# Kernel optimization log

Measured on AMD Instinct MI355X. Metric: run time of the kernel, lower is better.

Reference implementation:

```python
import jax, jax.numpy as jnp
import numpy as np

# Static configuration (matches init_kwargs)
EMBED_DIM = 256
NUM_HEADS = 8
NUM_LEVELS = 4
NUM_POINTS = 16
N_DEGREE = 3
HEAD_DIM = EMBED_DIM // NUM_HEADS
SPATIAL_SHAPES = ((64, 64), (32, 32), (16, 16), (8, 8))  # (H, W) per level
LEN_V = sum(h * w for h, w in SPATIAL_SHAPES)


def _bilinear_gather(v, loc, Hl, Wl):
    """Bilinear sampling with zero padding, align_corners=False.
    v:   [bs, nH, Hl*Wl, hd]  flattened level feature map (per head)
    loc: [bs, nH, Q, 2]       (x, y) in [0, 1]
    returns [bs, nH, Q, hd]
    """
    x = loc[..., 0] * Wl - 0.5
    y = loc[..., 1] * Hl - 0.5
    x0 = jnp.floor(x)
    y0 = jnp.floor(y)
    wx = x - x0
    wy = y - y0
    out = jnp.zeros(v.shape[:2] + (loc.shape[2], v.shape[-1]), v.dtype)
    corners = ((0, 0, (1 - wx) * (1 - wy)), (1, 0, wx * (1 - wy)),
               (0, 1, (1 - wx) * wy), (1, 1, wx * wy))
    for dx, dy, w in corners:
        xi = x0 + dx
        yi = y0 + dy
        valid = (xi >= 0) & (xi < Wl) & (yi >= 0) & (yi < Hl)
        idx = (jnp.clip(yi, 0, Hl - 1) * Wl + jnp.clip(xi, 0, Wl - 1)).astype(jnp.int32)
        g = jnp.take_along_axis(v, idx[..., None], axis=2)  # [bs,nH,Q,hd]
        out = out + g * (w * valid.astype(w.dtype))[..., None]
    return out


def setup_inputs() -> dict:
    key = jax.random.key(0)
    ks = jax.random.split(key, 12)
    bs, Lq = 4, 1024
    s = 0.02
    return {
        "query": jax.random.normal(ks[0], (bs, Lq, EMBED_DIM), jnp.float32),
        # polynomial coefficients for x(l), y(l); scaled so curves stay roughly in [0,1]
        "reference_points": jax.random.uniform(ks[1], (bs, Lq, 2 * (N_DEGREE + 1)), jnp.float32) * 0.25,
        "value": jax.random.normal(ks[2], (bs, LEN_V, EMBED_DIM), jnp.float32),
        "W_value": jax.random.normal(ks[3], (EMBED_DIM, EMBED_DIM), jnp.float32) * s,
        "b_value": jnp.zeros((EMBED_DIM,), jnp.float32),
        "W_offsets": jax.random.normal(ks[4], (EMBED_DIM, NUM_HEADS * NUM_LEVELS * NUM_POINTS * 2), jnp.float32) * s,
        "b_offsets": jax.random.normal(ks[5], (NUM_HEADS * NUM_LEVELS * NUM_POINTS * 2,), jnp.float32) * 0.5,
        "W_attn": jax.random.normal(ks[6], (EMBED_DIM, NUM_HEADS * NUM_LEVELS * NUM_POINTS), jnp.float32) * s,
        "b_attn": jnp.zeros((NUM_HEADS * NUM_LEVELS * NUM_POINTS,), jnp.float32),
        "W_out": jax.random.normal(ks[7], (EMBED_DIM, EMBED_DIM), jnp.float32) * s,
        "b_out": jnp.zeros((EMBED_DIM,), jnp.float32),
    }


def reference(query, reference_points, value, W_value, b_value, W_offsets,
              b_offsets, W_attn, b_attn, W_out, b_out):
    bs, Lq, _ = query.shape
    Lv = value.shape[1]
    nH, nL, nP, hd = NUM_HEADS, NUM_LEVELS, NUM_POINTS, HEAD_DIM

    v = (value @ W_value + b_value).reshape(bs, Lv, nH, hd)

    sampling_offsets = (query @ W_offsets + b_offsets).reshape(bs, Lq, nH, nL, nP, 2)
    attn = jax.nn.softmax((query @ W_attn + b_attn).reshape(bs, Lq, nH, nL * nP), axis=-1)
    attn = attn.reshape(bs, Lq, nH, nL, nP)

    # reference_points last dim == 8: polynomial branch
    lambdaz = jnp.linspace(0.0, 1.0, nP)
    lambdas = jnp.stack([lambdaz ** i for i in range(N_DEGREE, -1, -1)], axis=1)  # [nP, deg+1]
    ref_polys = reference_points.reshape(bs, Lq, 2, N_DEGREE + 1)
    pnts = jnp.einsum('bqcd,pd->bqpc', ref_polys, lambdas)  # [bs,Lq,nP,2] (x,y)

    # offset_normalizer: spatial shapes flipped -> (W, H) per level
    normalizer = jnp.array([[w, h] for (h, w) in SPATIAL_SHAPES], jnp.float32)
    normalizer = normalizer.reshape(1, 1, 1, nL, 1, 2)
    sampling_locations = pnts[:, :, None, None, :, :] + sampling_offsets / normalizer
    # -> [bs, Lq, nH, nL, nP, 2] in [0,1]

    # deformable attention core: per-level bilinear gather + softmax-weighted sum
    out = jnp.zeros((bs, Lq, nH, hd), v.dtype)
    start = 0
    for lvl, (Hl, Wl) in enumerate(SPATIAL_SHAPES):
        v_l = v[:, start:start + Hl * Wl].transpose(0, 2, 1, 3)  # [bs,nH,Hl*Wl,hd]
        loc_l = sampling_locations[:, :, :, lvl]                 # [bs,Lq,nH,nP,2]
        loc_l = loc_l.transpose(0, 2, 1, 3, 4).reshape(bs, nH, Lq * nP, 2)
        sampled = _bilinear_gather(v_l, loc_l, Hl, Wl).reshape(bs, nH, Lq, nP, hd)
        out = out + jnp.einsum('bhqpd,bqhp->bqhd', sampled, attn[:, :, :, lvl])
        start += Hl * Wl

    output = out.reshape(bs, Lq, nH * hd) @ W_out + b_out
    return output, sampling_locations, attn
```

## Files before the change

### kernel.cpp

```cpp
#include <hip/hip_runtime.h>
#include <math.h>

#define BS 4
#define LQ 1024
#define EMB 256
#define NH 8
#define NL 4
#define NP 16
#define HD 32
#define LV 5440
#define LVP 5936
#define KDIM 256

typedef __attribute__((ext_vector_type(8))) short short8;
typedef __attribute__((ext_vector_type(4))) float f32x4;

__device__ inline unsigned short f2bf(float f) {
    unsigned u = __builtin_bit_cast(unsigned, f);
    u += 0x7fff + ((u >> 16) & 1);
    return (unsigned short)(u >> 16);
}


__global__ __launch_bounds__(256) void prep(const float* __restrict__ Wv,
                                            const float* __restrict__ Wo,
                                            const float* __restrict__ Wa,
                                            const float* __restrict__ Wu,
                                            const float* __restrict__ value,
                                            const float* __restrict__ query,
                                            unsigned short* __restrict__ Wt,
                                            unsigned short* __restrict__ val_bf,
                                            unsigned short* __restrict__ qry_bf,
                                            unsigned short* __restrict__ v_pad) {
    const int blk = blockIdx.x;
    const int t = threadIdx.x;
    if (blk < 512) {
        __shared__ float tile[32][33];
        const int n0 = (blk & 63) * 32, k0 = (blk >> 6) * 32;
        const float* src; int N, nloc;
        if (n0 < 256)       { src = Wv; N = 256;  nloc = n0; }
        else if (n0 < 1280) { src = Wo; N = 1024; nloc = n0 - 256; }
        else if (n0 < 1792) { src = Wa; N = 512;  nloc = n0 - 1280; }
        else                { src = Wu; N = 256;  nloc = n0 - 1792; }
        const int tx = t & 31, ty = t >> 5;
#pragma unroll
        for (int i = 0; i < 32; i += 8)
            tile[ty + i][tx] = src[(size_t)(k0 + ty + i) * N + nloc + tx];
        __syncthreads();
        if (t < 128) {
            const int n_loc = t & 31, oct = t >> 5;
            const int n = n0 + n_loc;
            short8 h;
#pragma unroll
            for (int e = 0; e < 8; ++e) h[e] = (short)f2bf(tile[oct * 8 + e][n_loc]);
            const size_t off = ((size_t)(n >> 4) * 8 + (k0 >> 5)) * 512
                             + ((n & 15) + 16 * oct) * 8;
            *(short8*)(Wt + off) = h;
        }
    } else if (blk < 3744) {
        int i; const float* src; unsigned short* dst;
        if (blk < 3232) { i = (blk - 512) * 256 + t;  src = value; dst = val_bf; }
        else            { i = (blk - 3232) * 256 + t; src = query; dst = qry_bf; }
        const int r = i >> 5, oct = i & 31, k0 = oct * 8;
        const float4 f0 = *(const float4*)(src + (size_t)r * KDIM + k0);
        const float4 f1 = *(const float4*)(src + (size_t)r * KDIM + k0 + 4);
        short8 h;
        h[0] = (short)f2bf(f0.x); h[1] = (short)f2bf(f0.y);
        h[2] = (short)f2bf(f0.z); h[3] = (short)f2bf(f0.w);
        h[4] = (short)f2bf(f1.x); h[5] = (short)f2bf(f1.y);
        h[6] = (short)f2bf(f1.z); h[7] = (short)f2bf(f1.w);
        const size_t off = ((size_t)(r >> 4) * 8 + (oct >> 2)) * 512
                         + ((r & 15) + 16 * (oct & 3)) * 8;
        *(short8*)(dst + off) = h;
    } else {
        const int pidx = (blk - 3744) * 8 + (t >> 5);
        const int lane32 = t & 31;
        const unsigned b = (unsigned)pidx / 496u;
        const unsigned rem = (unsigned)pidx - b * 496u;
        int Wd, W2, pb, i;
        if (rem < 260)      { Wd = 64; W2 = 66; pb = 0;    i = rem; }
        else if (rem < 392) { Wd = 32; W2 = 34; pb = 4356; i = rem - 260; }
        else if (rem < 460) { Wd = 16; W2 = 18; pb = 5512; i = rem - 392; }
        else                { Wd = 8;  W2 = 10; pb = 5836; i = rem - 460; }
        int y, x;
        if (i < W2)          { y = 0;      x = i; }
        else if (i < 2 * W2) { y = Wd + 1; x = i - W2; }
        else { const int j = i - 2 * W2; y = 1 + (j >> 1); x = (j & 1) ? (Wd + 1) : 0; }
        const size_t off = ((size_t)b * LVP + pb + y * W2 + x) * EMB + lane32 * 8;
        uint4 z = {0, 0, 0, 0};
        *(uint4*)(v_pad + off) = z;
    }
}

template <int MODE>
__device__ __forceinline__ void gemm_nolds(const unsigned short* __restrict__ A,
                                           const unsigned short* __restrict__ Bt,
                                           const float* __restrict__ bias,
                                           const float* __restrict__ bias2,
                                           const float* __restrict__ refp,
                                           void* __restrict__ Cv,
                                           float* __restrict__ C2,
                                           int N, int bx, int by) {
    const int t = threadIdx.x;
    const int lane = t & 63, w = t >> 6;
    const int quad = lane >> 4, l16 = lane & 15;
    const int wr = w >> 1, wc = w & 1;
    const int row0 = by * 128, col0 = bx * 128;

    const unsigned short* ap = A  + ((size_t)((row0 >> 4) + wr * 4) * 8) * 512 + lane * 8;
    const unsigned short* bp = Bt + ((size_t)((col0 >> 4) + wc * 4) * 8) * 512 + lane * 8;

    f32x4 acc[4][4] = {};

#pragma unroll 2
    for (int kt = 0; kt < 8; ++kt) {
        short8 af[4], bf[4];
#pragma unroll
        for (int mi = 0; mi < 4; ++mi)
            af[mi] = *(const short8*)(ap + (size_t)mi * 4096 + kt * 512);
#pragma unroll
        for (int ni = 0; ni < 4; ++ni)
            bf[ni] = *(const short8*)(bp + (size_t)ni * 4096 + kt * 512);
#pragma unroll
        for (int mi = 0; mi < 4; ++mi)
#pragma unroll
            for (int ni = 0; ni < 4; ++ni)
                acc[mi][ni] = __builtin_amdgcn_mfma_f32_16x16x32_bf16(af[mi], bf[ni],
                                                                      acc[mi][ni], 0, 0, 0);
    }

    if (MODE == 0) {
#pragma unroll
        for (int ni = 0; ni < 4; ++ni) {
            const int c = col0 + wc * 64 + ni * 16 + l16;
            const float bv = bias[c];
#pragma unroll
            for (int mi = 0; mi < 4; ++mi) {
                const int r0 = row0 + wr * 64 + mi * 16 + quad * 4;
#pragma unroll
                for (int rr = 0; rr < 4; ++rr)
                    ((float*)Cv)[(size_t)(r0 + rr) * N + c] = acc[mi][ni][rr] + bv;
            }
        }
    } else if (MODE == 2) {
        unsigned short* C = (unsigned short*)Cv;
        float bv[4];
        int cc[4];
#pragma unroll
        for (int ni = 0; ni < 4; ++ni) {
            cc[ni] = col0 + wc * 64 + ni * 16 + l16;
            bv[ni] = bias[cc[ni]];
        }
#pragma unroll
        for (int mi = 0; mi < 4; ++mi) {
#pragma unroll
            for (int rr = 0; rr < 4; ++rr) {
                const unsigned r = row0 + wr * 64 + mi * 16 + quad * 4 + rr;
                const unsigned b = r / 5440u;
                const unsigned flat = r - b * 5440u;
                unsigned y, x, W2, pb;
                if (flat < 4096)      { y = flat >> 6; x = flat & 63; W2 = 66; pb = 0; }
                else if (flat < 5120) { const unsigned f = flat - 4096; y = f >> 5; x = f & 31; W2 = 34; pb = 4356; }
                else if (flat < 5376) { const unsigned f = flat - 5120; y = f >> 4; x = f & 15; W2 = 18; pb = 5512; }
                else                  { const unsigned f = flat - 5376; y = f >> 3; x = f & 7;  W2 = 10; pb = 5836; }
                const size_t rowbase = ((size_t)b * LVP + pb + (y + 1) * W2 + (x + 1)) * EMB;
#pragma unroll
                for (int ni = 0; ni < 4; ++ni)
                    C[rowbase + cc[ni]] = f2bf(acc[mi][ni][rr] + bv[ni]);
            }
        }
    } else {
        const bool is_off = (col0 < 1024);
        if (is_off) {
            float* C = (float*)Cv;
#pragma unroll
            for (int ni = 0; ni < 4; ++ni) {
                const int cg = col0 + wc * 64 + ni * 16 + l16;
                const int xy = cg & 1, p = (cg >> 1) & 15, l = (cg >> 5) & 3;
                const float lam = (float)p * (1.0f / 15.0f);
                const float l2 = lam * lam, l3 = l2 * lam;
                const float rW = (l == 0) ? 0.015625f : (l == 1) ? 0.03125f
                                : (l == 2) ? 0.0625f : 0.125f;
                const float bv = bias[cg];
#pragma unroll
                for (int mi = 0; mi < 4; ++mi) {
                    const int r0 = row0 + wr * 64 + mi * 16 + quad * 4;
#pragma unroll
                    for (int rr = 0; rr < 4; ++rr) {
                        const int r = r0 + rr;
                        const float4 rp = *(const float4*)(refp + (size_t)r * 8 + xy * 4);
                        const float poly = rp.x * l3 + rp.y * l2 + rp.z * lam + rp.w;
                        C[(size_t)r * 1024 + cg] = poly + (acc[mi][ni][rr] + bv) * rW;
                    }
                }
            }
        } else {
            const int cabase = col0 - 1024 + wc * 64;
            float bv[4];
#pragma unroll
            for (int ni = 0; ni < 4; ++ni) bv[ni] = bias2[cabase + ni * 16 + l16];
#pragma unroll
            for (int mi = 0; mi < 4; ++mi) {
                const int r0 = row0 + wr * 64 + mi * 16 + quad * 4;
#pragma unroll
                for (int rr = 0; rr < 4; ++rr) {
                    float v0 = acc[mi][0][rr] + bv[0];
                    float v1 = acc[mi][1][rr] + bv[1];
                    float v2 = acc[mi][2][rr] + bv[2];
                    float v3 = acc[mi][3][rr] + bv[3];
                    float mx = fmaxf(fmaxf(v0, v1), fmaxf(v2, v3));
#pragma unroll
                    for (int mk = 1; mk < 16; mk <<= 1) mx = fmaxf(mx, __shfl_xor(mx, mk));
                    v0 = __expf(v0 - mx); v1 = __expf(v1 - mx);
                    v2 = __expf(v2 - mx); v3 = __expf(v3 - mx);
                    float s = v0 + v1 + v2 + v3;
#pragma unroll
                    for (int mk = 1; mk < 16; mk <<= 1) s += __shfl_xor(s, mk);
                    const float inv = 1.0f / s;
                    const size_t rb = (size_t)(r0 + rr) * 512 + cabase + l16;
                    C2[rb]      = v0 * inv;
                    C2[rb + 16] = v1 * inv;
                    C2[rb + 32] = v2 * inv;
                    C2[rb + 48] = v3 * inv;
                }
            }
        }
    }
}

__global__ __launch_bounds__(256, 2) void gemm_fused(const unsigned short* __restrict__ val_bf,
                                                     const unsigned short* __restrict__ qry_bf,
                                                     const unsigned short* __restrict__ Wt,
                                                     const float* __restrict__ b_value,
                                                     const float* __restrict__ b_off,
                                                     const float* __restrict__ b_attn,
                                                     const float* __restrict__ refp,
                                                     unsigned short* __restrict__ v_pad,
                                                     float* __restrict__ loc_out,
                                                     float* __restrict__ attn_out) {
    const int b = blockIdx.x;
    if (b < 340) {
        gemm_nolds<2>(val_bf, Wt, b_value, nullptr, nullptr,
                      v_pad, nullptr, 256, b & 1, b >> 1);
    } else {
        const int b2 = b - 340;
        gemm_nolds<1>(qry_bf, Wt + (size_t)256 * KDIM, b_off, b_attn, refp,
                      loc_out, attn_out, 1536, b2 % 12, b2 / 12);
    }
}

__global__ __launch_bounds__(256, 2) void gemm_outp(const unsigned short* __restrict__ interm,
                                                    const unsigned short* __restrict__ Wt_out,
                                                    const float* __restrict__ b_out,
                                                    float* __restrict__ out) {
    gemm_nolds<0>(interm, Wt_out, b_out, nullptr, nullptr,
                  out, nullptr, 256, blockIdx.x & 1, blockIdx.x >> 1);
}

__global__ __launch_bounds__(256, 4) void sample_kernel(const unsigned short* __restrict__ v,
                                                        const float* __restrict__ loc,
                                                        const float* __restrict__ attn,
                                                        unsigned short* __restrict__ interm) {
    const int t = threadIdx.x;
    const int g = blockIdx.x * 16 + (t >> 4);
    const int l16i = t & 15;
    const int lvl = l16i >> 2;
    const int cq  = l16i & 3;
    const int h = g & 7, bq = g >> 3, b = bq >> 10;

    const int Wd = 64 >> lvl;
    const float Wf = (float)Wd;
    const int W2 = Wd + 2;
    const int rowoff = W2 * EMB;
    const int pb = (lvl == 0) ? 0 : (lvl == 1) ? 4356 : (lvl == 2) ? 5512 : 5836;

    const float* lp = loc  + (size_t)g * 128 + lvl * 32;
    const float* ap = attn + (size_t)g * 64  + lvl * 16;
    const unsigned short* vl = v + ((size_t)b * LVP + pb) * EMB + h * HD + cq * 8;

    float2 acc2[4] = {};

    auto cvt2 = [](unsigned d) {
        uint2 u; u.x = d << 16; u.y = d & 0xffff0000u;
        return __builtin_bit_cast(float2, u);
    };
    auto cadd = [&](const uint4 q, float wgt) {
        const float2 w2 = make_float2(wgt, wgt);
        acc2[0] += cvt2(q.x) * w2;
        acc2[1] += cvt2(q.y) * w2;
        acc2[2] += cvt2(q.z) * w2;
        acc2[3] += cvt2(q.w) * w2;
    };

    auto point = [&](float lx, float ly, float wt) {
        const float x = fmaf(lx, Wf, -0.5f);
        const float y = fmaf(ly, Wf, -0.5f);
        const float xc = fminf(fmaxf(x, -1.0f), Wf);
        const float yc = fminf(fmaxf(y, -1.0f), Wf);
        const float x0f = fminf(floorf(xc), Wf - 1.0f);
        const float y0f = fminf(floorf(yc), Wf - 1.0f);
        const float wx = xc - x0f, wy = yc - y0f;
        const float iwx = 1.0f - wx, iwy = 1.0f - wy;
        const int px = (int)x0f + 1;
        const int py = (int)y0f + 1;
        const int base = (py * W2 + px) * EMB;
        const float w00 = iwx * iwy * wt, w10 = wx * iwy * wt;
        const float w01 = iwx * wy * wt,  w11 = wx * wy * wt;
        const uint4 g00 = *(const uint4*)(vl + base);
        const uint4 g10 = *(const uint4*)(vl + base + EMB);
        const uint4 g01 = *(const uint4*)(vl + base + rowoff);
        const uint4 g11 = *(const uint4*)(vl + base + rowoff + EMB);
        cadd(g00, w00); cadd(g10, w10); cadd(g01, w01); cadd(g11, w11);
    };

#pragma unroll 1
    for (int p4 = 0; p4 < 16; p4 += 4) {
        const float4 la = *(const float4*)(lp + 2 * p4);
        const float4 lb = *(const float4*)(lp + 2 * p4 + 4);
        const float4 wv = *(const float4*)(ap + p4);
        point(la.x, la.y, wv.x); point(la.z, la.w, wv.y);
        point(lb.x, lb.y, wv.z); point(lb.z, lb.w, wv.w);
    }

    float a[8] = {acc2[0].x, acc2[0].y, acc2[1].x, acc2[1].y,
                  acc2[2].x, acc2[2].y, acc2[3].x, acc2[3].y};
#pragma unroll
    for (int m = 4; m <= 8; m <<= 1)
#pragma unroll
        for (int k = 0; k < 8; ++k) a[k] += __shfl_xor(a[k], m);

    if (lvl == 0) {
        unsigned short o[8];
#pragma unroll
        for (int k = 0; k < 8; ++k) o[k] = f2bf(a[k]);
        const size_t off = ((size_t)(bq >> 4) * 8 + h) * 512
                         + ((bq & 15) + 16 * cq) * 8;
        *(uint4*)(interm + off) = *(const uint4*)o;
    }
}

extern "C" void kernel_launch(void* const* d_in, const int* in_sizes, int n_in,
                              void* d_out, int out_size, void* d_ws, size_t ws_size,
                              hipStream_t stream) {
    const float* query   = (const float*)d_in[0];
    const float* refp    = (const float*)d_in[1];
    const float* value   = (const float*)d_in[2];
    const float* W_value = (const float*)d_in[3];
    const float* b_value = (const float*)d_in[4];
    const float* W_off   = (const float*)d_in[5];
    const float* b_off   = (const float*)d_in[6];
    const float* W_attn  = (const float*)d_in[7];
    const float* b_attn  = (const float*)d_in[8];
    const float* W_out   = (const float*)d_in[9];
    const float* b_out   = (const float*)d_in[10];

    float* out      = (float*)d_out;
    float* loc_out  = out + 1048576;
    float* attn_out = out + 5242880;

    char* ws = (char*)d_ws;
    unsigned short* v_pad  = (unsigned short*)ws;
    unsigned short* val_bf = (unsigned short*)(ws + 12156928);
    unsigned short* interm = (unsigned short*)(ws + 12156928);
    unsigned short* qry_bf = (unsigned short*)(ws + 23298048);
    unsigned short* Wt_all = (unsigned short*)(ws + 25395200);

    const dim3 blk(256);

    prep<<<3992, blk, 0, stream>>>(W_value, W_off, W_attn, W_out, value, query,
                                   Wt_all, val_bf, qry_bf, v_pad);

    gemm_fused<<<724, blk, 0, stream>>>(val_bf, qry_bf, Wt_all, b_value, b_off,
                                        b_attn, refp, v_pad, loc_out, attn_out);

    sample_kernel<<<(BS * LQ * NH) / 16, blk, 0, stream>>>(v_pad, loc_out, attn_out, interm);

    gemm_outp<<<64, blk, 0, stream>>>(interm, Wt_all + (size_t)1792 * KDIM, b_out, out);
}
```

Baseline: 166.4 us.

## Store padded value per-head contiguous and group sampling blocks by head

The padded bf16 value tensor changes from [b][pixel][256] to [head][b][pixel][32], so each head's 32-channel slice of a pixel and of neighbouring pixels sits in a compact region. The sampling kernel now assigns one head per block (blockIdx & 7) across 16 queries, so the blocks resident at once touch a single head's feature map. This is meant to give the bilinear gathers better cache locality and smaller strides. In exchange, the value-projection epilogue writes scattered 2-byte stores across head planes, which may cost more in the GEMM.

```diff
diff --git a/kernel.cpp b/kernel.cpp
--- a/kernel.cpp
+++ b/kernel.cpp
@@ -20,6 +20,7 @@
     u += 0x7fff + ((u >> 16) & 1);
     return (unsigned short)(u >> 16);
 }
+
 
 
 __global__ __launch_bounds__(256) void prep(const float* __restrict__ Wv,
@@ -86,7 +87,9 @@
         if (i < W2)          { y = 0;      x = i; }
         else if (i < 2 * W2) { y = Wd + 1; x = i - W2; }
         else { const int j = i - 2 * W2; y = 1 + (j >> 1); x = (j & 1) ? (Wd + 1) : 0; }
-        const size_t off = ((size_t)b * LVP + pb + y * W2 + x) * EMB + lane32 * 8;
+        const int hh = lane32 >> 2, cq = lane32 & 3;
+        const size_t off = (((size_t)(hh * BS + b) * LVP + pb + y * W2 + x) << 5)
+                         + cq * 8;
         uint4 z = {0, 0, 0, 0};
         *(uint4*)(v_pad + off) = z;
     }
@@ -163,10 +166,14 @@
                 else if (flat < 5120) { const unsigned f = flat - 4096; y = f >> 5; x = f & 31; W2 = 34; pb = 4356; }
                 else if (flat < 5376) { const unsigned f = flat - 5120; y = f >> 4; x = f & 15; W2 = 18; pb = 5512; }
                 else                  { const unsigned f = flat - 5376; y = f >> 3; x = f & 7;  W2 = 10; pb = 5836; }
-                const size_t rowbase = ((size_t)b * LVP + pb + (y + 1) * W2 + (x + 1)) * EMB;
-#pragma unroll
-                for (int ni = 0; ni < 4; ++ni)
-                    C[rowbase + cc[ni]] = f2bf(acc[mi][ni][rr] + bv[ni]);
+                const size_t pix = (size_t)(pb + (y + 1) * W2 + (x + 1)) << 5;
+#pragma unroll
+                for (int ni = 0; ni < 4; ++ni) {
+                    const int cc_ = cc[ni];
+                    const size_t off = (((size_t)((cc_ >> 5) * BS + b) * LVP) << 5)
+                                     + pix + (cc_ & 31);
+                    C[off] = f2bf(acc[mi][ni][rr] + bv[ni]);
+                }
             }
         }
     } else {
@@ -262,21 +269,23 @@
                                                         const float* __restrict__ attn,
                                                         unsigned short* __restrict__ interm) {
     const int t = threadIdx.x;
-    const int g = blockIdx.x * 16 + (t >> 4);
+    const int h = blockIdx.x & 7;
+    const int bq = (blockIdx.x >> 3) * 16 + (t >> 4);
     const int l16i = t & 15;
     const int lvl = l16i >> 2;
     const int cq  = l16i & 3;
-    const int h = g & 7, bq = g >> 3, b = bq >> 10;
+    const int b = bq >> 10;
+    const int g = bq * 8 + h;
 
     const int Wd = 64 >> lvl;
     const float Wf = (float)Wd;
     const int W2 = Wd + 2;
-    const int rowoff = W2 * EMB;
+    const int rowoff = W2 * 32;
     const int pb = (lvl == 0) ? 0 : (lvl == 1) ? 4356 : (lvl == 2) ? 5512 : 5836;
 
     const float* lp = loc  + (size_t)g * 128 + lvl * 32;
     const float* ap = attn + (size_t)g * 64  + lvl * 16;
-    const unsigned short* vl = v + ((size_t)b * LVP + pb) * EMB + h * HD + cq * 8;
+    const unsigned short* vl = v + (((size_t)(h * BS + b) * LVP + pb) << 5) + cq * 8;
 
     float2 acc2[4] = {};
 
@@ -303,13 +312,13 @@
         const float iwx = 1.0f - wx, iwy = 1.0f - wy;
         const int px = (int)x0f + 1;
         const int py = (int)y0f + 1;
-        const int base = (py * W2 + px) * EMB;
+        const int base = (py * W2 + px) << 5;
         const float w00 = iwx * iwy * wt, w10 = wx * iwy * wt;
         const float w01 = iwx * wy * wt,  w11 = wx * wy * wt;
         const uint4 g00 = *(const uint4*)(vl + base);
-        const uint4 g10 = *(const uint4*)(vl + base + EMB);
+        const uint4 g10 = *(const uint4*)(vl + base + 32);
         const uint4 g01 = *(const uint4*)(vl + base + rowoff);
-        const uint4 g11 = *(const uint4*)(vl + base + rowoff + EMB);
+        const uint4 g11 = *(const uint4*)(vl + base + rowoff + 32);
         cadd(g00, w00); cadd(g10, w10); cadd(g01, w01); cadd(g11, w11);
     };
 
```

After: 155.7 us. 6.4% less time.
